# Kernel optimization log

Measured on AMD Instinct MI355X. Metric: run time of the kernel, lower is better.

Reference implementation:

```python
import jax, jax.numpy as jnp
import numpy as np

TOP_K = 8
N_EXPERTS = 256
N_GROUP = 8
TOPK_GROUP = 4
SCALE = 2.5


def setup_inputs() -> dict:
    key = jax.random.key(0)
    k1, k2, k3 = jax.random.split(key, 3)
    hidden_states = jax.random.normal(k1, (4, 2048, 7168), dtype=jnp.float32)
    weight = jax.random.normal(k2, (N_EXPERTS, 7168), dtype=jnp.float32) * 0.02
    e_score_correction_bias = jax.random.normal(k3, (N_EXPERTS,), dtype=jnp.float32) * 0.1
    return {"hidden_states": hidden_states, "weight": weight,
            "e_score_correction_bias": e_score_correction_bias}


def reference(hidden_states, weight, e_score_correction_bias):
    B, S, H = hidden_states.shape
    x = hidden_states.reshape(-1, H).astype(jnp.float32)          # [T, H]
    router_logits = jnp.einsum('th,eh->te', x, weight)            # [T, E]
    scores = jax.nn.sigmoid(router_logits)                        # [T, E]
    scores_b = scores + e_score_correction_bias[None, :]          # bias-corrected
    T = x.shape[0]
    # per-group score = sum of top-2 bias-corrected scores in the group
    grouped = scores_b.reshape(T, N_GROUP, N_EXPERTS // N_GROUP)
    group_scores = jax.lax.top_k(grouped, 2)[0].sum(-1)           # [T, G]
    group_idx = jax.lax.top_k(group_scores, TOPK_GROUP)[1]        # [T, topk_group]
    group_mask = jax.nn.one_hot(group_idx, N_GROUP, dtype=jnp.bool_).any(axis=1)  # [T, G]
    expert_mask = jnp.repeat(group_mask, N_EXPERTS // N_GROUP, axis=-1)           # [T, E]
    masked = jnp.where(expert_mask, scores_b, -jnp.inf)
    _, topk_indices = jax.lax.top_k(masked, TOP_K)                # [T, top_k]
    topk_weights = jnp.take_along_axis(scores, topk_indices, axis=-1)  # un-biased scores
    topk_weights = topk_weights / jnp.sum(topk_weights, axis=-1, keepdims=True)
    topk_weights = topk_weights * SCALE
    return topk_indices, topk_weights
```

## Files before the change

### kernel.cpp

```cpp
#include <hip/hip_runtime.h>
#include <math.h>

typedef __attribute__((ext_vector_type(4))) float f32x4;
typedef _Float16 f16;
typedef __attribute__((ext_vector_type(8))) _Float16 f16x8;

constexpr int H       = 7168;
constexpr int E       = 256;
constexpr int T_TOTAL = 8192;

constexpr int KSPLIT  = 4;
constexpr int K_SLICE = H / KSPLIT;
constexpr int NCH     = K_SLICE / 64;
constexpr int NPAIR   = NCH / 2;
constexpr int NKC     = K_SLICE / 32;
constexpr int MT      = 64;

constexpr int N_GROUP    = 8;
constexpr int TOPK_GROUP = 4;
constexpr int TOP_K      = 8;

constexpr size_t SCORES_OFF = 8u * 1024 * 1024;

__global__ __launch_bounds__(64) void pack_w_kernel(const float* __restrict__ w,
                                                    f16* __restrict__ wf)
{
    const int l  = threadIdx.x;
    const int nt = blockIdx.x & 15;
    const int kc = blockIdx.x >> 4;
    const int e  = nt * 16 + (l & 15);
    const int h  = kc * 32 + (l >> 4) * 8;
    const float* src = &w[(size_t)e * H + h];
    f32x4 v0 = *reinterpret_cast<const f32x4*>(src);
    f32x4 v1 = *reinterpret_cast<const f32x4*>(src + 4);
    float v[8] = {v0[0], v0[1], v0[2], v0[3], v1[0], v1[1], v1[2], v1[3]};
    f16x8 hi, lo;
    #pragma unroll
    for (int j = 0; j < 8; ++j) {
        f16 h16 = (f16)v[j];
        hi[j] = h16;
        lo[j] = (f16)(v[j] - (float)h16);
    }
    const size_t base = (((size_t)kc * 16 + nt) * 2) * 512 + (size_t)l * 8;
    *reinterpret_cast<f16x8*>(&wf[base])       = hi;
    *reinterpret_cast<f16x8*>(&wf[base + 512]) = lo;
}

__global__ __launch_bounds__(512, 4) void gemm_kernel(
    const float* __restrict__ x,
    const f16*   __restrict__ wf,
    float* __restrict__ scores)
{
    __shared__ __align__(16) f16 x_lds[2][2][4 * 2 * 2 * 512];

    const int tid  = threadIdx.x;
    const int lane = tid & 63;
    const int wn   = tid >> 6;

    const int bid = blockIdx.x;
    const int ksl = bid & 3;
    const int mb  = bid >> 2;
    const int t0  = mb * MT;
    const int k0  = ksl * K_SLICE;
    const int kc0 = k0 >> 5;

    const int lmt = (tid >> 6) & 3;
    const int lks = tid >> 8;
    const float* xrow = &x[(size_t)(t0 + lmt * 16 + (lane & 15)) * H
                           + k0 + lks * 32 + (lane >> 4) * 8];

    const int lm = lane & 15;
    const int kq = lane >> 4;

    f32x4 acc[4][2];
    #pragma unroll
    for (int mt = 0; mt < 4; ++mt)
        #pragma unroll
        for (int nt = 0; nt < 2; ++nt)
            acc[mt][nt] = (f32x4){0.f, 0.f, 0.f, 0.f};

    auto stage = [&](int bu, int half, f32x4 v0, f32x4 v1) {
        float v[8] = {v0[0], v0[1], v0[2], v0[3], v1[0], v1[1], v1[2], v1[3]};
        f16x8 hi, lo;
        #pragma unroll
        for (int j = 0; j < 8; ++j) {
            f16 h16 = (f16)v[j];
            hi[j] = h16;
            lo[j] = (f16)(v[j] - (float)h16);
        }
        f16* base = &x_lds[bu][half][((lmt * 2 + lks) * 2) * 512 + lane * 8];
        *reinterpret_cast<f16x8*>(base)       = hi;
        *reinterpret_cast<f16x8*>(base + 512) = lo;
    };

    auto load_b = [&](f16x8 (&b)[2][2], int kc) {
        #pragma unroll
        for (int nt = 0; nt < 2; ++nt)
            #pragma unroll
            for (int s = 0; s < 2; ++s)
                b[nt][s] = *reinterpret_cast<const f16x8*>(
                    &wf[(((size_t)kc * 16 + wn * 2 + nt) * 2 + s) * 512 + lane * 8]);
    };

    auto mfma_step = [&](const f16x8 (&b)[2][2], int bu, int half, int ks) {
        #pragma unroll
        for (int mt = 0; mt < 4; ++mt) {
            const f16* ap = &x_lds[bu][half][((mt * 2 + ks) * 2) * 512 + lane * 8];
            f16x8 ahi = *reinterpret_cast<const f16x8*>(ap);
            f16x8 alo = *reinterpret_cast<const f16x8*>(ap + 512);
            acc[mt][0] = __builtin_amdgcn_mfma_f32_16x16x32_f16(ahi, b[0][0], acc[mt][0], 0, 0, 0);
            acc[mt][1] = __builtin_amdgcn_mfma_f32_16x16x32_f16(ahi, b[1][0], acc[mt][1], 0, 0, 0);
            acc[mt][0] = __builtin_amdgcn_mfma_f32_16x16x32_f16(ahi, b[0][1], acc[mt][0], 0, 0, 0);
            acc[mt][1] = __builtin_amdgcn_mfma_f32_16x16x32_f16(ahi, b[1][1], acc[mt][1], 0, 0, 0);
            acc[mt][0] = __builtin_amdgcn_mfma_f32_16x16x32_f16(alo, b[0][0], acc[mt][0], 0, 0, 0);
            acc[mt][1] = __builtin_amdgcn_mfma_f32_16x16x32_f16(alo, b[1][0], acc[mt][1], 0, 0, 0);
        }
    };

    f16x8 B0[2][2], B1[2][2], B2[2][2], B3[2][2];

    {
        f32x4 v0 = *reinterpret_cast<const f32x4*>(xrow);
        f32x4 v1 = *reinterpret_cast<const f32x4*>(xrow + 4);
        f32x4 v2 = *reinterpret_cast<const f32x4*>(xrow + 64);
        f32x4 v3 = *reinterpret_cast<const f32x4*>(xrow + 68);
        stage(0, 0, v0, v1);
        stage(0, 1, v2, v3);
    }
    load_b(B0, kc0);
    load_b(B1, kc0 + 1);
    load_b(B2, kc0 + 2);
    __syncthreads();

    for (int i = 0; i < NPAIR; ++i) {
        const int buf   = i & 1;
        const int g     = i * 4;
        const int kbase = kc0 + g;
        const bool last = (i + 1 == NPAIR);

        f32x4 nva0, nva1, nvb0, nvb1;
        if (!last) {
            const float* nx = xrow + (2 * i + 2) * 64;
            nva0 = *reinterpret_cast<const f32x4*>(nx);
            nva1 = *reinterpret_cast<const f32x4*>(nx + 4);
            nvb0 = *reinterpret_cast<const f32x4*>(nx + 64);
            nvb1 = *reinterpret_cast<const f32x4*>(nx + 68);
        }

        __builtin_amdgcn_s_setprio(1);
        load_b(B3, (g + 3 < NKC) ? (kbase + 3) : kc0);
        mfma_step(B0, buf, 0, 0);
        load_b(B0, (g + 4 < NKC) ? (kbase + 4) : kc0);
        mfma_step(B1, buf, 0, 1);
        load_b(B1, (g + 5 < NKC) ? (kbase + 5) : kc0);
        mfma_step(B2, buf, 1, 0);
        load_b(B2, (g + 6 < NKC) ? (kbase + 6) : kc0);
        mfma_step(B3, buf, 1, 1);
        __builtin_amdgcn_s_setprio(0);

        if (!last) {
            stage(buf ^ 1, 0, nva0, nva1);
            stage(buf ^ 1, 1, nvb0, nvb1);
            asm volatile("s_waitcnt lgkmcnt(0)" ::: "memory");
            __builtin_amdgcn_s_barrier();
            asm volatile("" ::: "memory");
        }
    }

    #pragma unroll
    for (int mt = 0; mt < 4; ++mt)
        #pragma unroll
        for (int nt = 0; nt < 2; ++nt)
            #pragma unroll
            for (int r = 0; r < 4; ++r) {
                const int tok = mt * 16 + kq * 4 + r;
                const int e   = wn * 32 + nt * 16 + lm;
                scores[(((size_t)(t0 + tok)) * KSPLIT + ksl) * E + e] = acc[mt][nt][r];
            }
}

__global__ __launch_bounds__(256) void gate_kernel(
    const float* __restrict__ scores,
    const float* __restrict__ bias,
    float* __restrict__ out)
{
    const int lane = threadIdx.x & 63;
    const int wv   = threadIdx.x >> 6;
    const int t    = blockIdx.x * 4 + wv;

    const float* p = &scores[(size_t)t * (KSPLIT * E) + lane * 4];
    f32x4 s = (f32x4){0.f, 0.f, 0.f, 0.f};
    #pragma unroll
    for (int k = 0; k < KSPLIT; ++k)
        s += *reinterpret_cast<const f32x4*>(p + k * E);
    f32x4 bi = *reinterpret_cast<const f32x4*>(&bias[lane * 4]);

    float sig[4], bsc[4];
    #pragma unroll
    for (int j = 0; j < 4; ++j) {
        sig[j] = 1.0f / (1.0f + expf(-s[j]));
        bsc[j] = sig[j] + bi[j];
    }

    float h01 = fmaxf(bsc[0], bsc[1]), l01 = fminf(bsc[0], bsc[1]);
    float h23 = fmaxf(bsc[2], bsc[3]), l23 = fminf(bsc[2], bsc[3]);
    float m1 = fmaxf(h01, h23);
    float m2 = fmaxf(fminf(h01, h23), fmaxf(l01, l23));
    #pragma unroll
    for (int d = 1; d < 8; d <<= 1) {
        float om1 = __shfl_xor(m1, d);
        float om2 = __shfl_xor(m2, d);
        float nm1 = fmaxf(m1, om1);
        float nm2 = fmaxf(fminf(m1, om1), fmaxf(m2, om2));
        m1 = nm1; m2 = nm2;
    }
    const float gs  = m1 + m2;
    const int   gid = lane >> 3;

    int cnt = 0;
    #pragma unroll
    for (int j = 0; j < N_GROUP; ++j) {
        float gsj = __shfl(gs, j * 8);
        cnt += (gsj > gs || (gsj == gs && j < gid)) ? 1 : 0;
    }
    const bool sel = (cnt < TOPK_GROUP);

    float mb[4];
    #pragma unroll
    for (int j = 0; j < 4; ++j) mb[j] = sel ? bsc[j] : -INFINITY;

    float wsum = 0.f;
    f32x4 iv0, iv1, wv0, wv1;
    #pragma unroll
    for (int r = 0; r < TOP_K; ++r) {
        float v = mb[0]; int li = 0;
        if (mb[1] > v) { v = mb[1]; li = 1; }
        if (mb[2] > v) { v = mb[2]; li = 2; }
        if (mb[3] > v) { v = mb[3]; li = 3; }
        int ei = lane * 4 + li;
        #pragma unroll
        for (int d = 1; d < 64; d <<= 1) {
            float ov = __shfl_xor(v, d);
            int   oi = __shfl_xor(ei, d);
            if (ov > v || (ov == v && oi < ei)) { v = ov; ei = oi; }
        }
        const int sub = ei & 3, owner = ei >> 2;
        const float svl = (sub & 2) ? ((sub & 1) ? sig[3] : sig[2])
                                    : ((sub & 1) ? sig[1] : sig[0]);
        const float wr = __shfl(svl, owner);
        #pragma unroll
        for (int j = 0; j < 4; ++j)
            if (lane == owner && j == sub) mb[j] = -INFINITY;
        wsum += wr;
        if (r < 4) { iv0[r] = (float)ei;     wv0[r] = wr; }
        else       { iv1[r - 4] = (float)ei; wv1[r - 4] = wr; }
    }

    const float scale = 2.5f / wsum;
    #pragma unroll
    for (int j = 0; j < 4; ++j) { wv0[j] *= scale; wv1[j] *= scale; }

    if (lane == 0) {
        float* oi_ = out + (size_t)t * TOP_K;
        float* ow_ = out + (size_t)T_TOTAL * TOP_K + (size_t)t * TOP_K;
        *reinterpret_cast<f32x4*>(oi_)     = iv0;
        *reinterpret_cast<f32x4*>(oi_ + 4) = iv1;
        *reinterpret_cast<f32x4*>(ow_)     = wv0;
        *reinterpret_cast<f32x4*>(ow_ + 4) = wv1;
    }
}

extern "C" void kernel_launch(void* const* d_in, const int* in_sizes, int n_in,
                              void* d_out, int out_size, void* d_ws, size_t ws_size,
                              hipStream_t stream) {
    const float* x    = (const float*)d_in[0];
    const float* w    = (const float*)d_in[1];
    const float* bias = (const float*)d_in[2];
    float* out = (float*)d_out;

    f16*   wf     = (f16*)d_ws;
    float* scores = (float*)((char*)d_ws + SCORES_OFF);

    hipLaunchKernelGGL(pack_w_kernel, dim3((H / 32) * 16), dim3(64), 0, stream, w, wf);
    hipLaunchKernelGGL(gemm_kernel, dim3((T_TOTAL / MT) * KSPLIT), dim3(512), 0, stream,
                       x, wf, scores);
    hipLaunchKernelGGL(gate_kernel, dim3(T_TOTAL / 4), dim3(256), 0, stream,
                       scores, bias, out);
}
```

Before: 366.8 us.

## Fuse weight fp16 hi/lo split into GEMM, dropping the pack kernel

Removes the separate pack_w kernel and has the GEMM load fp32 weight rows directly, converting them to fp16 hi/lo pairs in registers just before the MFMAs. The B prefetch pipeline changes from three-deep packed fp16 to a two-stage raw load plus convert. This saves one kernel launch and the write and reread of the packed weight buffer. In exchange every block repeats the conversion VALU work, reads weights from global memory as strided fp32 rows instead of contiguous fragments, and has a shallower prefetch.

```diff
diff --git a/kernel.cpp b/kernel.cpp
--- a/kernel.cpp
+++ b/kernel.cpp
@@ -22,33 +22,9 @@
 
 constexpr size_t SCORES_OFF = 8u * 1024 * 1024;
 
-__global__ __launch_bounds__(64) void pack_w_kernel(const float* __restrict__ w,
-                                                    f16* __restrict__ wf)
-{
-    const int l  = threadIdx.x;
-    const int nt = blockIdx.x & 15;
-    const int kc = blockIdx.x >> 4;
-    const int e  = nt * 16 + (l & 15);
-    const int h  = kc * 32 + (l >> 4) * 8;
-    const float* src = &w[(size_t)e * H + h];
-    f32x4 v0 = *reinterpret_cast<const f32x4*>(src);
-    f32x4 v1 = *reinterpret_cast<const f32x4*>(src + 4);
-    float v[8] = {v0[0], v0[1], v0[2], v0[3], v1[0], v1[1], v1[2], v1[3]};
-    f16x8 hi, lo;
-    #pragma unroll
-    for (int j = 0; j < 8; ++j) {
-        f16 h16 = (f16)v[j];
-        hi[j] = h16;
-        lo[j] = (f16)(v[j] - (float)h16);
-    }
-    const size_t base = (((size_t)kc * 16 + nt) * 2) * 512 + (size_t)l * 8;
-    *reinterpret_cast<f16x8*>(&wf[base])       = hi;
-    *reinterpret_cast<f16x8*>(&wf[base + 512]) = lo;
-}
-
 __global__ __launch_bounds__(512, 4) void gemm_kernel(
     const float* __restrict__ x,
-    const f16*   __restrict__ wf,
+    const float* __restrict__ w,
     float* __restrict__ scores)
 {
     __shared__ __align__(16) f16 x_lds[2][2][4 * 2 * 2 * 512];
@@ -72,6 +48,9 @@
     const int lm = lane & 15;
     const int kq = lane >> 4;
 
+    const float* wrow0 = &w[(size_t)(wn * 32 + 0  + lm) * H + (lane >> 4) * 8];
+    const float* wrow1 = &w[(size_t)(wn * 32 + 16 + lm) * H + (lane >> 4) * 8];
+
     f32x4 acc[4][2];
     #pragma unroll
     for (int mt = 0; mt < 4; ++mt)
@@ -93,13 +72,25 @@
         *reinterpret_cast<f16x8*>(base + 512) = lo;
     };
 
-    auto load_b = [&](f16x8 (&b)[2][2], int kc) {
+    auto load_raw = [&](f32x4 (&r)[2][2], int kc) {
+        const float* s0 = wrow0 + (size_t)kc * 32;
+        const float* s1 = wrow1 + (size_t)kc * 32;
+        r[0][0] = *reinterpret_cast<const f32x4*>(s0);
+        r[0][1] = *reinterpret_cast<const f32x4*>(s0 + 4);
+        r[1][0] = *reinterpret_cast<const f32x4*>(s1);
+        r[1][1] = *reinterpret_cast<const f32x4*>(s1 + 4);
+    };
+
+    auto cvt_b = [&](const f32x4 (&r)[2][2], f16x8 (&b)[2][2]) {
         #pragma unroll
         for (int nt = 0; nt < 2; ++nt)
             #pragma unroll
-            for (int s = 0; s < 2; ++s)
-                b[nt][s] = *reinterpret_cast<const f16x8*>(
-                    &wf[(((size_t)kc * 16 + wn * 2 + nt) * 2 + s) * 512 + lane * 8]);
+            for (int j = 0; j < 8; ++j) {
+                float v = (j < 4) ? r[nt][0][j] : r[nt][1][j - 4];
+                f16 h16 = (f16)v;
+                b[nt][0][j] = h16;
+                b[nt][1][j] = (f16)(v - (float)h16);
+            }
     };
 
     auto mfma_step = [&](const f16x8 (&b)[2][2], int bu, int half, int ks) {
@@ -117,7 +108,8 @@
         }
     };
 
-    f16x8 B0[2][2], B1[2][2], B2[2][2], B3[2][2];
+    f32x4 R0[2][2], R1[2][2];
+    f16x8 F0[2][2], F1[2][2];
 
     {
         f32x4 v0 = *reinterpret_cast<const f32x4*>(xrow);
@@ -127,9 +119,9 @@
         stage(0, 0, v0, v1);
         stage(0, 1, v2, v3);
     }
-    load_b(B0, kc0);
-    load_b(B1, kc0 + 1);
-    load_b(B2, kc0 + 2);
+    load_raw(R0, kc0);
+    load_raw(R1, kc0 + 1);
+    cvt_b(R0, F0);
     __syncthreads();
 
     for (int i = 0; i < NPAIR; ++i) {
@@ -148,14 +140,18 @@
         }
 
         __builtin_amdgcn_s_setprio(1);
-        load_b(B3, (g + 3 < NKC) ? (kbase + 3) : kc0);
-        mfma_step(B0, buf, 0, 0);
-        load_b(B0, (g + 4 < NKC) ? (kbase + 4) : kc0);
-        mfma_step(B1, buf, 0, 1);
-        load_b(B1, (g + 5 < NKC) ? (kbase + 5) : kc0);
-        mfma_step(B2, buf, 1, 0);
-        load_b(B2, (g + 6 < NKC) ? (kbase + 6) : kc0);
-        mfma_step(B3, buf, 1, 1);
+        load_raw(R0, (g + 2 < NKC) ? (kbase + 2) : kc0);
+        cvt_b(R1, F1);
+        mfma_step(F0, buf, 0, 0);
+        load_raw(R1, (g + 3 < NKC) ? (kbase + 3) : kc0);
+        cvt_b(R0, F0);
+        mfma_step(F1, buf, 0, 1);
+        load_raw(R0, (g + 4 < NKC) ? (kbase + 4) : kc0);
+        cvt_b(R1, F1);
+        mfma_step(F0, buf, 1, 0);
+        load_raw(R1, (g + 5 < NKC) ? (kbase + 5) : kc0);
+        cvt_b(R0, F0);
+        mfma_step(F1, buf, 1, 1);
         __builtin_amdgcn_s_setprio(0);
 
         if (!last) {
@@ -278,12 +274,10 @@
     const float* bias = (const float*)d_in[2];
     float* out = (float*)d_out;
 
-    f16*   wf     = (f16*)d_ws;
     float* scores = (float*)((char*)d_ws + SCORES_OFF);
 
-    hipLaunchKernelGGL(pack_w_kernel, dim3((H / 32) * 16), dim3(64), 0, stream, w, wf);
     hipLaunchKernelGGL(gemm_kernel, dim3((T_TOTAL / MT) * KSPLIT), dim3(512), 0, stream,
-                       x, wf, scores);
+                       x, w, scores);
     hipLaunchKernelGGL(gate_kernel, dim3(T_TOTAL / 4), dim3(256), 0, stream,
                        scores, bias, out);
 }
```

New measurement: 410.5 us. +11.9%, slower.
